# Kernel tuning notes

Measured on AMD Instinct MI355X. Metric: run time of the kernel, lower is better.

Reference implementation:

```python
import jax, jax.numpy as jnp
import numpy as np

LN_EPS = 1e-5      # torch nn.LayerNorm default
NORM_EPS = 1e-12   # torch F.normalize default


def _layer_norm(x, gamma, beta):
    mu = jnp.mean(x, axis=-1, keepdims=True)
    var = jnp.mean((x - mu) ** 2, axis=-1, keepdims=True)
    return (x - mu) * jax.lax.rsqrt(var + LN_EPS) * gamma + beta


def _l2_normalize_rows(w):
    n = jnp.sqrt(jnp.sum(w * w, axis=1, keepdims=True))
    return w / jnp.maximum(n, NORM_EPS)


def setup_inputs() -> dict:
    key = jax.random.key(0)
    B, D = 32768, 512
    ks = jax.random.split(key, 4)
    return {
        "stimulus": jax.random.normal(ks[0], (B, D), dtype=jnp.float32),
        "prev_activation": jax.random.normal(ks[1], (B, D), dtype=jnp.float32),
        "W": jax.random.normal(ks[2], (D, D), dtype=jnp.float32),
        "Wr": jax.random.normal(ks[3], (D, D), dtype=jnp.float32),
        "alpha": jnp.full((D,), 0.1, dtype=jnp.float32),
        "decay": jnp.full((D,), 0.01, dtype=jnp.float32),
        "ln_act_gamma": jnp.ones((D,), dtype=jnp.float32),
        "ln_act_beta": jnp.zeros((D,), dtype=jnp.float32),
        "ln_rec_gamma": jnp.ones((D,), dtype=jnp.float32),
        "ln_rec_beta": jnp.zeros((D,), dtype=jnp.float32),
    }


def reference(stimulus, prev_activation, W, Wr, alpha, decay,
              ln_act_gamma, ln_act_beta, ln_rec_gamma, ln_rec_beta):
    # recurrent path
    rec_out = prev_activation @ Wr                      # [B, D]
    rec_norm = _layer_norm(rec_out, ln_rec_gamma, ln_rec_beta)
    # stimulus path
    stim_out = stimulus @ W                             # [B, D]
    final = jax.nn.relu(stim_out + rec_norm)
    final = _layer_norm(final, ln_act_gamma, ln_act_beta)

    # Hebbian weight update (detached in the original module)
    heb_upd = jnp.einsum('bi,bj->ij', stimulus, stim_out) * alpha[None, :]
    rec_upd = jnp.einsum('bi,bj->ij', prev_activation, rec_out) * alpha[None, :]
    # diag(decay) @ W is a row-wise broadcast scale
    new_W = _l2_normalize_rows(W + heb_upd - decay[:, None] * W)
    new_Wr = _l2_normalize_rows(Wr + rec_upd - decay[:, None] * Wr)

    return final, new_W, new_Wr
```

## Files before the change

kernel.cpp:

```cpp
#include <hip/hip_runtime.h>
#include <stdint.h>

typedef unsigned int u32;
typedef unsigned short u16;
typedef float  f32x4 __attribute__((ext_vector_type(4)));
typedef u32    u32x4 __attribute__((ext_vector_type(4)));
typedef __bf16 bf16x8 __attribute__((ext_vector_type(8)));

static __device__ __forceinline__ u16 f2bf(float f){
  u32 u = __builtin_bit_cast(u32, f);
  return (u16)((u + 0x7FFFu + ((u >> 16) & 1u)) >> 16);
}

static __device__ __forceinline__ void async16(const void* g, void* l){
  __builtin_amdgcn_global_load_lds((const __attribute__((address_space(1))) u32*)g,
                                   (__attribute__((address_space(3))) u32*)l, 16, 0, 0);
}

static __device__ __forceinline__ float wave_sum(float v){
#pragma unroll
  for (int o = 32; o > 0; o >>= 1) v += __shfl_xor(v, o, 64);
  return v;
}

__global__ __launch_bounds__(256) void k_cvt(const float* __restrict__ s0, const float* __restrict__ s1,
                                             u16* __restrict__ d0, u16* __restrict__ d1){
  const float* __restrict__ src = blockIdx.y ? s1 : s0;
  u16* __restrict__ dst = blockIdx.y ? d1 : d0;
  size_t i = ((size_t)blockIdx.x*256 + threadIdx.x) * 8;
  f32x4 a = *(const f32x4*)(src + i);
  f32x4 b = *(const f32x4*)(src + i + 4);
  u32x4 w;
  w[0] = (u32)f2bf(a[0]) | ((u32)f2bf(a[1]) << 16);
  w[1] = (u32)f2bf(a[2]) | ((u32)f2bf(a[3]) << 16);
  w[2] = (u32)f2bf(b[0]) | ((u32)f2bf(b[1]) << 16);
  w[3] = (u32)f2bf(b[2]) | ((u32)f2bf(b[3]) << 16);
  *(u32x4*)(dst + i) = w;
}

__global__ __launch_bounds__(256) void k_tcvt(const float* __restrict__ s0, const float* __restrict__ s1,
                                              u16* __restrict__ d0, u16* __restrict__ d1,
                                              int R, int C){
  const float* __restrict__ src = blockIdx.z ? s1 : s0;
  u16* __restrict__ dst = blockIdx.z ? d1 : d0;
  __shared__ u16 lt[64*72];
  const int c0 = blockIdx.x * 64, r0 = blockIdx.y * 64;
  const int tid = threadIdx.x;
  const int rr = tid >> 4, c4 = tid & 15;
#pragma unroll
  for (int p = 0; p < 4; ++p){
    int r = rr + p*16;
    f32x4 f = *(const f32x4*)(src + (size_t)(r0 + r)*C + c0 + c4*4);
#pragma unroll
    for (int e = 0; e < 4; ++e) lt[(c4*4 + e)*72 + r] = f2bf(f[e]);
  }
  __syncthreads();
  const int c = tid >> 2, bg = tid & 3;
  const u32x4* lp = (const u32x4*)(lt + c*72 + bg*16);
  u32x4 w0 = lp[0], w1 = lp[1];
  u16* drow = dst + (size_t)(c0 + c)*R + r0 + bg*16;
  *(u32x4*)drow = w0;
  *(u32x4*)(drow + 8) = w1;
}

__global__ __launch_bounds__(512) void k_gemm_fwd(const u16* __restrict__ SN, const u16* __restrict__ PN,
                                                  const u16* __restrict__ Wt, const u16* __restrict__ Wrt,
                                                  u16* __restrict__ SO, u16* __restrict__ RO,
                                                  u16* __restrict__ SOT, u16* __restrict__ ROT){
  __shared__ char smem[67584];
  u16* sA = (u16*)smem;
  u16* sB = (u16*)(smem + 32768);
  const int tid = threadIdx.x;
  const int lane = tid & 63, wid = tid >> 6;
  const int wm = wid >> 1, wn = wid & 1;
  const int l15 = lane & 15, q = lane >> 4;
  const int id = blockIdx.x;
  const int c8 = id & 7, g = id >> 3;
  const int sel = g >> 6, h = g & 63;
  const int yb = c8*16 + (h >> 2), xb = h & 3;
  const int m0 = yb * 256, n0 = xb * 128;
  const u16* __restrict__ A  = sel ? PN  : SN;
  const u16* __restrict__ Bt = sel ? Wrt : Wt;
  u16* __restrict__ Cn = sel ? RO  : SO;
  u16* __restrict__ Ct = sel ? ROT : SOT;

  f32x4 acc[4][4];
  const f32x4 vzero = {0.f, 0.f, 0.f, 0.f};
#pragma unroll
  for (int a = 0; a < 4; ++a)
#pragma unroll
    for (int b = 0; b < 4; ++b) acc[a][b] = vzero;

#pragma unroll 1
  for (int kt = 0; kt < 8; ++kt){
    const int k0 = kt*64;
#pragma unroll
    for (int it = 0; it < 4; ++it){
      int gg0 = it*512 + tid;
      int r = gg0 >> 3, gp = gg0 & 7, gsw = gp ^ (r & 7);
      async16(A + (size_t)(m0 + r)*512 + k0 + gsw*8, (char*)sA + (size_t)gg0*16);
    }
#pragma unroll
    for (int it = 0; it < 2; ++it){
      int gg0 = it*512 + tid;
      int r = gg0 >> 3, gp = gg0 & 7, gsw = gp ^ (r & 7);
      async16(Bt + (size_t)(n0 + r)*512 + k0 + gsw*8, (char*)sB + (size_t)gg0*16);
    }
    __syncthreads();
#pragma unroll
    for (int kk = 0; kk < 2; ++kk){
      bf16x8 af[4], bfv[4];
#pragma unroll
      for (int mt = 0; mt < 4; ++mt){
        int r = wm*64 + mt*16 + l15;
        int gsw = (kk*4 + q) ^ (r & 7);
        af[mt] = *(const bf16x8*)(sA + (size_t)(r*8 + gsw)*8);
      }
#pragma unroll
      for (int nt = 0; nt < 4; ++nt){
        int r = wn*64 + nt*16 + l15;
        int gsw = (kk*4 + q) ^ (r & 7);
        bfv[nt] = *(const bf16x8*)(sB + (size_t)(r*8 + gsw)*8);
      }
#pragma unroll
      for (int mt = 0; mt < 4; ++mt)
#pragma unroll
        for (int nt = 0; nt < 4; ++nt)
          acc[mt][nt] = __builtin_amdgcn_mfma_f32_16x16x32_bf16(af[mt], bfv[nt], acc[mt][nt], 0, 0, 0);
    }
    __syncthreads();
  }

  u16* lt = (u16*)smem;
#pragma unroll
  for (int mt = 0; mt < 4; ++mt)
#pragma unroll
    for (int nt = 0; nt < 4; ++nt){
      f32x4 v = acc[mt][nt];
      u16 b0 = f2bf(v[0]), b1 = f2bf(v[1]), b2 = f2bf(v[2]), b3 = f2bf(v[3]);
      int n = wn*64 + nt*16 + l15;
      int mb = wm*64 + mt*16 + q*4;
      u16* cn = Cn + (size_t)(m0 + mb)*512 + n0 + n;
      cn[0] = b0; cn[512] = b1; cn[1024] = b2; cn[1536] = b3;
      *(u32*)(lt + n*264 + mb)     = (u32)b0 | ((u32)b1 << 16);
      *(u32*)(lt + n*264 + mb + 2) = (u32)b2 | ((u32)b3 << 16);
    }
  __syncthreads();
#pragma unroll
  for (int p = 0; p < 8; ++p){
    int gg0 = p*512 + tid;
    int n = gg0 >> 5, mg = gg0 & 31;
    u32x4 w = *(const u32x4*)(lt + n*264 + mg*8);
    *(u32x4*)(Ct + (size_t)(n0 + n)*32768 + m0 + mg*8) = w;
  }
}

__global__ __launch_bounds__(512) void k_gemm_upd(const u16* __restrict__ A0, const u16* __restrict__ B0,
                                                  const u16* __restrict__ A1, const u16* __restrict__ B1,
                                                  float* __restrict__ part){
  __shared__ char smem[67584];
  char* sAn = smem;
  u32*  sAt = (u32*)(smem + 16384);
  u16*  sB  = (u16*)(smem + 34816);
  const int tid = threadIdx.x;
  const int lane = tid & 63, wid = tid >> 6;
  const int wm = wid >> 2, wn = wid & 3;
  const int l15 = lane & 15, q = lane >> 4;
  const int id = blockIdx.x;
  const int c8 = id & 7, g = id >> 3;
  const int zz = c8*8 + (g >> 3);
  const int xy = g & 7;
  const int mat = zz >> 5, sp = zz & 31;
  const int yb = xy & 3, xb = xy >> 2;
  const u16* __restrict__ A = mat ? A1 : A0;
  const u16* __restrict__ B = mat ? B1 : B0;
  const int m0 = yb * 128, n0 = xb * 256;
  const int kb = sp * 1024;
  const int base_c = tid >> 5, pr = tid & 31;
  const int ce = (base_c + pr) & 15;

  f32x4 acc[4][4];
  const f32x4 vzero = {0.f, 0.f, 0.f, 0.f};
#pragma unroll
  for (int a = 0; a < 4; ++a)
#pragma unroll
    for (int b = 0; b < 4; ++b) acc[a][b] = vzero;

#pragma unroll 1
  for (int kt = 0; kt < 16; ++kt){
    const int k0 = kb + kt*64;
#pragma unroll
    for (int it = 0; it < 2; ++it){
      int gg0 = it*512 + tid;
      int r = gg0 >> 4, gp = gg0 & 15;
      async16(A + (size_t)(k0 + r)*512 + m0 + gp*8, sAn + (size_t)gg0*16);
    }
#pragma unroll
    for (int it = 0; it < 4; ++it){
      int gg0 = it*512 + tid;
      int r = gg0 >> 3, gp = gg0 & 7, gsw = gp ^ (r & 7);
      async16(B + (size_t)(n0 + r)*32768 + k0 + gsw*8, (char*)sB + (size_t)gg0*16);
    }
    __syncthreads();
    {
      u32x4 r0 = *(const u32x4*)(sAn + (size_t)(2*pr)*256 + ce*16);
      u32x4 r1 = *(const u32x4*)(sAn + (size_t)(2*pr)*256 + 256 + ce*16);
#pragma unroll
      for (int e = 0; e < 4; ++e){
        u32 lo = r0[e], hi = r1[e];
        sAt[(ce*8 + 2*e    )*36 + pr] = (lo & 0xFFFFu) | (hi << 16);
        sAt[(ce*8 + 2*e + 1)*36 + pr] = (lo >> 16) | (hi & 0xFFFF0000u);
      }
    }
    __syncthreads();
#pragma unroll
    for (int kk = 0; kk < 2; ++kk){
      bf16x8 af[4], bfv[4];
#pragma unroll
      for (int mt = 0; mt < 4; ++mt){
        int r = wm*64 + mt*16 + l15;
        af[mt] = *(const bf16x8*)(sAt + (size_t)r*36 + kk*16 + q*4);
      }
#pragma unroll
      for (int nt = 0; nt < 4; ++nt){
        int r = wn*64 + nt*16 + l15;
        int gsw = (kk*4 + q) ^ (r & 7);
        bfv[nt] = *(const bf16x8*)(sB + (size_t)(r*8 + gsw)*8);
      }
#pragma unroll
      for (int mt = 0; mt < 4; ++mt)
#pragma unroll
        for (int nt = 0; nt < 4; ++nt)
          acc[mt][nt] = __builtin_amdgcn_mfma_f32_16x16x32_bf16(af[mt], bfv[nt], acc[mt][nt], 0, 0, 0);
    }
    __syncthreads();
  }

  float* dst = part + (size_t)(mat*32 + sp)*262144;
#pragma unroll
  for (int mt = 0; mt < 4; ++mt)
#pragma unroll
    for (int nt = 0; nt < 4; ++nt){
      f32x4 v = acc[mt][nt];
      int n = wn*64 + nt*16 + l15;
      int mb = wm*64 + mt*16 + q*4;
      float* d = dst + (size_t)(m0 + mb)*512 + n0 + n;
      d[0] = v[0]; d[512] = v[1]; d[1024] = v[2]; d[1536] = v[3];
    }
}

__global__ __launch_bounds__(256) void k_ln(const u16* __restrict__ SO, const u16* __restrict__ RO,
                                            const float* __restrict__ ga, const float* __restrict__ ba,
                                            const float* __restrict__ gr, const float* __restrict__ br,
                                            float* __restrict__ out){
  const int wid = threadIdx.x >> 6, lane = threadIdx.x & 63;
  const size_t b = (size_t)blockIdx.x*4 + wid;
  const int c = lane*8;
  float x[8], t[8];
  {
    u32x4 u = *(const u32x4*)(RO + b*512 + c);
#pragma unroll
    for (int i = 0; i < 4; ++i){
      u32 w = u[i];
      x[2*i]   = __uint_as_float(w << 16);
      x[2*i+1] = __uint_as_float(w & 0xFFFF0000u);
    }
  }
  float s = 0.f, ss = 0.f;
#pragma unroll
  for (int e = 0; e < 8; ++e){ s += x[e]; ss += x[e]*x[e]; }
  s = wave_sum(s); ss = wave_sum(ss);
  float mu = s*(1.f/512.f);
  float var = fmaxf(ss*(1.f/512.f) - mu*mu, 0.f);
  float rs = rsqrtf(var + 1e-5f);
  f32x4 g0 = *(const f32x4*)(gr + c), g1 = *(const f32x4*)(gr + c + 4);
  f32x4 h0 = *(const f32x4*)(br + c), h1 = *(const f32x4*)(br + c + 4);
  {
    u32x4 u = *(const u32x4*)(SO + b*512 + c);
    float so[8];
#pragma unroll
    for (int i = 0; i < 4; ++i){
      u32 w = u[i];
      so[2*i]   = __uint_as_float(w << 16);
      so[2*i+1] = __uint_as_float(w & 0xFFFF0000u);
    }
#pragma unroll
    for (int e = 0; e < 4; ++e) t[e]   = fmaxf(so[e]   + (x[e]  -mu)*rs*g0[e] + h0[e], 0.f);
#pragma unroll
    for (int e = 0; e < 4; ++e) t[4+e] = fmaxf(so[4+e] + (x[4+e]-mu)*rs*g1[e] + h1[e], 0.f);
  }
  float s2 = 0.f, ss2 = 0.f;
#pragma unroll
  for (int e = 0; e < 8; ++e){ s2 += t[e]; ss2 += t[e]*t[e]; }
  s2 = wave_sum(s2); ss2 = wave_sum(ss2);
  float mu2 = s2*(1.f/512.f);
  float var2 = fmaxf(ss2*(1.f/512.f) - mu2*mu2, 0.f);
  float rs2 = rsqrtf(var2 + 1e-5f);
  f32x4 G0 = *(const f32x4*)(ga + c), G1 = *(const f32x4*)(ga + c + 4);
  f32x4 H0 = *(const f32x4*)(ba + c), H1 = *(const f32x4*)(ba + c + 4);
  f32x4 o0, o1;
#pragma unroll
  for (int e = 0; e < 4; ++e){
    o0[e] = (t[e]   - mu2)*rs2*G0[e] + H0[e];
    o1[e] = (t[4+e] - mu2)*rs2*G1[e] + H1[e];
  }
  *(f32x4*)(out + b*512 + c)     = o0;
  *(f32x4*)(out + b*512 + c + 4) = o1;
}

__global__ __launch_bounds__(256) void k_finalize(const float* __restrict__ W0, const float* __restrict__ W1,
                                                  const float* __restrict__ part,
                                                  const float* __restrict__ alpha, const float* __restrict__ decay,
                                                  float* __restrict__ out){
  const int i = blockIdx.x, mat = blockIdx.y;
  const int t = threadIdx.x;
  const float* Wm = mat ? W1 : W0;
  const float* pb = part + (size_t)mat*32*262144 + (size_t)i*512;
  const float dc = decay[i];
  float v[2], ssq = 0.f;
#pragma unroll
  for (int h = 0; h < 2; ++h){
    int j = t + h*256;
    float acc = 0.f;
#pragma unroll
    for (int sp = 0; sp < 32; ++sp) acc += pb[(size_t)sp*262144 + j];
    float val = Wm[(size_t)i*512 + j]*(1.f - dc) + alpha[j]*acc;
    v[h] = val; ssq += val*val;
  }
  float wsum = wave_sum(ssq);
  __shared__ float red[4];
  const int lane = t & 63, wid = t >> 6;
  if (lane == 0) red[wid] = wsum;
  __syncthreads();
  float tot = red[0] + red[1] + red[2] + red[3];
  float rn = 1.f / fmaxf(sqrtf(tot), 1e-12f);
  out[(size_t)mat*262144 + (size_t)i*512 + t]       = v[0]*rn;
  out[(size_t)mat*262144 + (size_t)i*512 + t + 256] = v[1]*rn;
}

extern "C" void kernel_launch(void* const* d_in, const int* in_sizes, int n_in,
                              void* d_out, int out_size, void* d_ws, size_t ws_size,
                              hipStream_t stream) {
  const float* S  = (const float*)d_in[0];
  const float* P  = (const float*)d_in[1];
  const float* W  = (const float*)d_in[2];
  const float* Wr = (const float*)d_in[3];
  const float* alpha = (const float*)d_in[4];
  const float* decay = (const float*)d_in[5];
  const float* ga = (const float*)d_in[6];
  const float* ba = (const float*)d_in[7];
  const float* gr = (const float*)d_in[8];
  const float* br = (const float*)d_in[9];
  float* out = (float*)d_out;

  char* ws = (char*)d_ws;
  u16* SN  = (u16*)(ws);
  u16* PN  = (u16*)(ws + 33554432);
  u16* SOT = (u16*)(ws + 67108864);
  u16* ROT = (u16*)(ws + 100663296);
  u16* SO  = (u16*)(ws + 134217728);
  u16* RO  = (u16*)(ws + 167772160);
  u16* Wt  = (u16*)(ws + 201326592);
  u16* Wrt = (u16*)(ws + 201850880);
  float* part = (float*)(ws + 134217728);

  k_cvt<<<dim3(8192, 2), dim3(256), 0, stream>>>(S, P, SN, PN);
  k_tcvt<<<dim3(8, 8, 2), dim3(256), 0, stream>>>(W, Wr, Wt, Wrt, 512, 512);
  k_gemm_fwd<<<dim3(1024), dim3(512), 0, stream>>>(SN, PN, Wt, Wrt, SO, RO, SOT, ROT);
  k_ln<<<dim3(8192), dim3(256), 0, stream>>>(SO, RO, ga, ba, gr, br, out);
  k_gemm_upd<<<dim3(512), dim3(512), 0, stream>>>(SN, SOT, PN, ROT, part);
  k_finalize<<<dim3(512, 2), dim3(256), 0, stream>>>(W, Wr, part, alpha, decay, out + 16777216);
}
```

Before: 317.5 us.

## Pre-transpose bf16 activations so the update GEMM skips its in-LDS transpose

The conversion kernel now also writes a transposed bf16 copy of stimulus and prev_activation when the workspace is large enough. If it is not, a separate transpose kernel produces that copy after the layernorm. The update GEMM then loads A tiles K-contiguous with the same XOR swizzle as B. This removes the per-tile LDS transpose pass and one barrier, and cuts LDS use. The cost is extra global traffic to write and read 64 MB of transposed activations, and the workspace layout is reorganised to fit both paths.

```diff
diff --git a/kernel.cpp b/kernel.cpp
--- a/kernel.cpp
+++ b/kernel.cpp
@@ -23,19 +23,71 @@
   return v;
 }
 
-__global__ __launch_bounds__(256) void k_cvt(const float* __restrict__ s0, const float* __restrict__ s1,
-                                             u16* __restrict__ d0, u16* __restrict__ d1){
-  const float* __restrict__ src = blockIdx.y ? s1 : s0;
-  u16* __restrict__ dst = blockIdx.y ? d1 : d0;
-  size_t i = ((size_t)blockIdx.x*256 + threadIdx.x) * 8;
-  f32x4 a = *(const f32x4*)(src + i);
-  f32x4 b = *(const f32x4*)(src + i + 4);
-  u32x4 w;
-  w[0] = (u32)f2bf(a[0]) | ((u32)f2bf(a[1]) << 16);
-  w[1] = (u32)f2bf(a[2]) | ((u32)f2bf(a[3]) << 16);
-  w[2] = (u32)f2bf(b[0]) | ((u32)f2bf(b[1]) << 16);
-  w[3] = (u32)f2bf(b[2]) | ((u32)f2bf(b[3]) << 16);
-  *(u32x4*)(dst + i) = w;
+__global__ __launch_bounds__(256) void k_cvt2(const float* __restrict__ s0, const float* __restrict__ s1,
+                                              u16* __restrict__ dn0, u16* __restrict__ dn1,
+                                              u16* __restrict__ dt0, u16* __restrict__ dt1,
+                                              int wn, int wt){
+  const float* __restrict__ src = blockIdx.z ? s1 : s0;
+  u16* __restrict__ dn = blockIdx.z ? dn1 : dn0;
+  u16* __restrict__ dt = blockIdx.z ? dt1 : dt0;
+  __shared__ u16 lt[64*72];
+  const int c0 = blockIdx.x * 64;
+  const int r0 = blockIdx.y * 64;
+  const int tid = threadIdx.x;
+  const int rr = tid >> 4, c4 = tid & 15;
+#pragma unroll
+  for (int p = 0; p < 4; ++p){
+    int r = rr + p*16;
+    f32x4 f = *(const f32x4*)(src + (size_t)(r0 + r)*512 + c0 + c4*4);
+    u16 b0 = f2bf(f[0]), b1 = f2bf(f[1]), b2 = f2bf(f[2]), b3 = f2bf(f[3]);
+    if (wt){
+      lt[(c4*4 + 0)*72 + r] = b0;
+      lt[(c4*4 + 1)*72 + r] = b1;
+      lt[(c4*4 + 2)*72 + r] = b2;
+      lt[(c4*4 + 3)*72 + r] = b3;
+    }
+    if (wn){
+      u32* qp = (u32*)(dn + (size_t)(r0 + r)*512 + c0 + c4*4);
+      qp[0] = (u32)b0 | ((u32)b1 << 16);
+      qp[1] = (u32)b2 | ((u32)b3 << 16);
+    }
+  }
+  if (!wt) return;
+  __syncthreads();
+  const int c = tid >> 2, bg = tid & 3;
+  const u32x4* lp = (const u32x4*)(lt + c*72 + bg*16);
+  u32x4 w0 = lp[0], w1 = lp[1];
+  u16* drow = dt + (size_t)(c0 + c)*32768 + r0 + bg*16;
+  *(u32x4*)drow = w0;
+  *(u32x4*)(drow + 8) = w1;
+}
+
+__global__ __launch_bounds__(256) void k_tpose(const u16* __restrict__ s0, const u16* __restrict__ s1,
+                                               u16* __restrict__ d0, u16* __restrict__ d1){
+  const u16* __restrict__ src = blockIdx.z ? s1 : s0;
+  u16* __restrict__ dst = blockIdx.z ? d1 : d0;
+  __shared__ u16 lt[64*72];
+  const int c0 = blockIdx.x * 64, r0 = blockIdx.y * 64;
+  const int tid = threadIdx.x;
+  const int rr = tid >> 3, c8 = tid & 7;
+#pragma unroll
+  for (int p = 0; p < 2; ++p){
+    int r = rr + p*32;
+    u32x4 w = *(const u32x4*)(src + (size_t)(r0 + r)*512 + c0 + c8*8);
+#pragma unroll
+    for (int e = 0; e < 4; ++e){
+      u32 v = w[e];
+      lt[(c8*8 + 2*e    )*72 + r] = (u16)(v & 0xFFFFu);
+      lt[(c8*8 + 2*e + 1)*72 + r] = (u16)(v >> 16);
+    }
+  }
+  __syncthreads();
+  const int c = tid >> 2, bg = tid & 3;
+  const u32x4* lp = (const u32x4*)(lt + c*72 + bg*16);
+  u32x4 w0 = lp[0], w1 = lp[1];
+  u16* drow = dst + (size_t)(c0 + c)*32768 + r0 + bg*16;
+  *(u32x4*)drow = w0;
+  *(u32x4*)(drow + 8) = w1;
 }
 
 __global__ __launch_bounds__(256) void k_tcvt(const float* __restrict__ s0, const float* __restrict__ s1,
@@ -158,10 +210,9 @@
 __global__ __launch_bounds__(512) void k_gemm_upd(const u16* __restrict__ A0, const u16* __restrict__ B0,
                                                   const u16* __restrict__ A1, const u16* __restrict__ B1,
                                                   float* __restrict__ part){
-  __shared__ char smem[67584];
-  char* sAn = smem;
-  u32*  sAt = (u32*)(smem + 16384);
-  u16*  sB  = (u16*)(smem + 34816);
+  __shared__ char smem[49152];
+  u16* sA = (u16*)smem;
+  u16* sB = (u16*)(smem + 16384);
   const int tid = threadIdx.x;
   const int lane = tid & 63, wid = tid >> 6;
   const int wm = wid >> 2, wn = wid & 3;
@@ -176,8 +227,6 @@
   const u16* __restrict__ B = mat ? B1 : B0;
   const int m0 = yb * 128, n0 = xb * 256;
   const int kb = sp * 1024;
-  const int base_c = tid >> 5, pr = tid & 31;
-  const int ce = (base_c + pr) & 15;
 
   f32x4 acc[4][4];
   const f32x4 vzero = {0.f, 0.f, 0.f, 0.f};
@@ -192,8 +241,8 @@
 #pragma unroll
     for (int it = 0; it < 2; ++it){
       int gg0 = it*512 + tid;
-      int r = gg0 >> 4, gp = gg0 & 15;
-      async16(A + (size_t)(k0 + r)*512 + m0 + gp*8, sAn + (size_t)gg0*16);
+      int r = gg0 >> 3, gp = gg0 & 7, gsw = gp ^ (r & 7);
+      async16(A + (size_t)(m0 + r)*32768 + k0 + gsw*8, (char*)sA + (size_t)gg0*16);
     }
 #pragma unroll
     for (int it = 0; it < 4; ++it){
@@ -202,24 +251,14 @@
       async16(B + (size_t)(n0 + r)*32768 + k0 + gsw*8, (char*)sB + (size_t)gg0*16);
     }
     __syncthreads();
-    {
-      u32x4 r0 = *(const u32x4*)(sAn + (size_t)(2*pr)*256 + ce*16);
-      u32x4 r1 = *(const u32x4*)(sAn + (size_t)(2*pr)*256 + 256 + ce*16);
-#pragma unroll
-      for (int e = 0; e < 4; ++e){
-        u32 lo = r0[e], hi = r1[e];
-        sAt[(ce*8 + 2*e    )*36 + pr] = (lo & 0xFFFFu) | (hi << 16);
-        sAt[(ce*8 + 2*e + 1)*36 + pr] = (lo >> 16) | (hi & 0xFFFF0000u);
-      }
-    }
-    __syncthreads();
 #pragma unroll
     for (int kk = 0; kk < 2; ++kk){
       bf16x8 af[4], bfv[4];
 #pragma unroll
       for (int mt = 0; mt < 4; ++mt){
         int r = wm*64 + mt*16 + l15;
-        af[mt] = *(const bf16x8*)(sAt + (size_t)r*36 + kk*16 + q*4);
+        int gsw = (kk*4 + q) ^ (r & 7);
+        af[mt] = *(const bf16x8*)(sA + (size_t)(r*8 + gsw)*8);
       }
 #pragma unroll
       for (int nt = 0; nt < 4; ++nt){
@@ -354,20 +393,41 @@
   float* out = (float*)d_out;
 
   char* ws = (char*)d_ws;
-  u16* SN  = (u16*)(ws);
-  u16* PN  = (u16*)(ws + 33554432);
-  u16* SOT = (u16*)(ws + 67108864);
-  u16* ROT = (u16*)(ws + 100663296);
-  u16* SO  = (u16*)(ws + 134217728);
-  u16* RO  = (u16*)(ws + 167772160);
-  u16* Wt  = (u16*)(ws + 201326592);
-  u16* Wrt = (u16*)(ws + 201850880);
-  float* part = (float*)(ws + 134217728);
-
-  k_cvt<<<dim3(8192, 2), dim3(256), 0, stream>>>(S, P, SN, PN);
+  const size_t M32 = 33554432;
+  const bool big = ws_size >= (size_t)269484032;
+
+  u16 *SN, *PN, *ST, *PT, *SOT, *ROT, *SO, *RO, *Wt, *Wrt;
+  if (big){
+    SN  = (u16*)(ws);
+    PN  = (u16*)(ws + 1*M32);
+    ST  = (u16*)(ws + 2*M32);
+    PT  = (u16*)(ws + 3*M32);
+    SOT = (u16*)(ws + 4*M32);
+    ROT = (u16*)(ws + 5*M32);
+    SO  = (u16*)(ws + 6*M32);
+    RO  = (u16*)(ws + 7*M32);
+    Wt  = (u16*)(ws + 8*M32);
+    Wrt = (u16*)(ws + 8*M32 + 524288);
+  } else {
+    SN  = (u16*)(ws);
+    PN  = (u16*)(ws + 1*M32);
+    SOT = (u16*)(ws + 2*M32);
+    ROT = (u16*)(ws + 3*M32);
+    SO  = (u16*)(ws + 4*M32);
+    RO  = (u16*)(ws + 5*M32);
+    Wt  = (u16*)(ws + 6*M32);
+    Wrt = (u16*)(ws + 6*M32 + 524288);
+    ST  = SO;
+    PT  = RO;
+  }
+  float* part = (float*)ws;
+
+  k_cvt2<<<dim3(8, 512, 2), dim3(256), 0, stream>>>(S, P, SN, PN, ST, PT, 1, big ? 1 : 0);
   k_tcvt<<<dim3(8, 8, 2), dim3(256), 0, stream>>>(W, Wr, Wt, Wrt, 512, 512);
   k_gemm_fwd<<<dim3(1024), dim3(512), 0, stream>>>(SN, PN, Wt, Wrt, SO, RO, SOT, ROT);
   k_ln<<<dim3(8192), dim3(256), 0, stream>>>(SO, RO, ga, ba, gr, br, out);
-  k_gemm_upd<<<dim3(512), dim3(512), 0, stream>>>(SN, SOT, PN, ROT, part);
+  if (!big)
+    k_tpose<<<dim3(8, 512, 2), dim3(256), 0, stream>>>(SN, PN, ST, PT);
+  k_gemm_upd<<<dim3(512), dim3(512), 0, stream>>>(ST, SOT, PT, ROT, part);
   k_finalize<<<dim3(512, 2), dim3(256), 0, stream>>>(W, Wr, part, alpha, decay, out + 16777216);
 }
```

After: 347.7 us. 9.5% more time.

## Fuse fp32-to-bf16 input conversion into both GEMM A-operand loads

Applied to the files above, without the earlier changes.

Removes the standalone conversion kernel for stimulus and prev_activation. Both GEMMs now load fp32 rows directly into registers, pack them to bf16 and store them to LDS. This avoids writing and re-reading bf16 copies of the large inputs and saves one launch. In exchange, the GEMMs read twice as many bytes per A tile, and the A operand no longer uses the direct global-to-LDS async path.

```diff
diff --git a/kernel.cpp b/kernel.cpp
--- a/kernel.cpp
+++ b/kernel.cpp
@@ -12,35 +12,28 @@
   return (u16)((u + 0x7FFFu + ((u >> 16) & 1u)) >> 16);
 }
 
-static __device__ __forceinline__ void async16(const void* g, void* l){
-  __builtin_amdgcn_global_load_lds((const __attribute__((address_space(1))) u32*)g,
-                                   (__attribute__((address_space(3))) u32*)l, 16, 0, 0);
-}
-
-static __device__ __forceinline__ float wave_sum(float v){
-#pragma unroll
-  for (int o = 32; o > 0; o >>= 1) v += __shfl_xor(v, o, 64);
-  return v;
-}
-
-__global__ __launch_bounds__(256) void k_cvt(const float* __restrict__ s0, const float* __restrict__ s1,
-                                             u16* __restrict__ d0, u16* __restrict__ d1){
-  const float* __restrict__ src = blockIdx.y ? s1 : s0;
-  u16* __restrict__ dst = blockIdx.y ? d1 : d0;
-  size_t i = ((size_t)blockIdx.x*256 + threadIdx.x) * 8;
-  f32x4 a = *(const f32x4*)(src + i);
-  f32x4 b = *(const f32x4*)(src + i + 4);
+static __device__ __forceinline__ u32x4 pack8(f32x4 a, f32x4 b){
   u32x4 w;
   w[0] = (u32)f2bf(a[0]) | ((u32)f2bf(a[1]) << 16);
   w[1] = (u32)f2bf(a[2]) | ((u32)f2bf(a[3]) << 16);
   w[2] = (u32)f2bf(b[0]) | ((u32)f2bf(b[1]) << 16);
   w[3] = (u32)f2bf(b[2]) | ((u32)f2bf(b[3]) << 16);
-  *(u32x4*)(dst + i) = w;
-}
-
-__global__ __launch_bounds__(256) void k_tcvt(const float* __restrict__ s0, const float* __restrict__ s1,
-                                              u16* __restrict__ d0, u16* __restrict__ d1,
-                                              int R, int C){
+  return w;
+}
+
+static __device__ __forceinline__ void async16(const void* g, void* l){
+  __builtin_amdgcn_global_load_lds((const __attribute__((address_space(1))) u32*)g,
+                                   (__attribute__((address_space(3))) u32*)l, 16, 0, 0);
+}
+
+static __device__ __forceinline__ float wave_sum(float v){
+#pragma unroll
+  for (int o = 32; o > 0; o >>= 1) v += __shfl_xor(v, o, 64);
+  return v;
+}
+
+__global__ __launch_bounds__(256) void k_wcvt(const float* __restrict__ s0, const float* __restrict__ s1,
+                                              u16* __restrict__ d0, u16* __restrict__ d1){
   const float* __restrict__ src = blockIdx.z ? s1 : s0;
   u16* __restrict__ dst = blockIdx.z ? d1 : d0;
   __shared__ u16 lt[64*72];
@@ -50,7 +43,7 @@
 #pragma unroll
   for (int p = 0; p < 4; ++p){
     int r = rr + p*16;
-    f32x4 f = *(const f32x4*)(src + (size_t)(r0 + r)*C + c0 + c4*4);
+    f32x4 f = *(const f32x4*)(src + (size_t)(r0 + r)*512 + c0 + c4*4);
 #pragma unroll
     for (int e = 0; e < 4; ++e) lt[(c4*4 + e)*72 + r] = f2bf(f[e]);
   }
@@ -58,12 +51,12 @@
   const int c = tid >> 2, bg = tid & 3;
   const u32x4* lp = (const u32x4*)(lt + c*72 + bg*16);
   u32x4 w0 = lp[0], w1 = lp[1];
-  u16* drow = dst + (size_t)(c0 + c)*R + r0 + bg*16;
+  u16* drow = dst + (size_t)(c0 + c)*512 + r0 + bg*16;
   *(u32x4*)drow = w0;
   *(u32x4*)(drow + 8) = w1;
 }
 
-__global__ __launch_bounds__(512) void k_gemm_fwd(const u16* __restrict__ SN, const u16* __restrict__ PN,
+__global__ __launch_bounds__(512) void k_gemm_fwd(const float* __restrict__ Sf, const float* __restrict__ Pf,
                                                   const u16* __restrict__ Wt, const u16* __restrict__ Wrt,
                                                   u16* __restrict__ SO, u16* __restrict__ RO,
                                                   u16* __restrict__ SOT, u16* __restrict__ ROT){
@@ -79,8 +72,8 @@
   const int sel = g >> 6, h = g & 63;
   const int yb = c8*16 + (h >> 2), xb = h & 3;
   const int m0 = yb * 256, n0 = xb * 128;
-  const u16* __restrict__ A  = sel ? PN  : SN;
-  const u16* __restrict__ Bt = sel ? Wrt : Wt;
+  const float* __restrict__ A = sel ? Pf  : Sf;
+  const u16* __restrict__ Bt  = sel ? Wrt : Wt;
   u16* __restrict__ Cn = sel ? RO  : SO;
   u16* __restrict__ Ct = sel ? ROT : SOT;
 
@@ -94,17 +87,25 @@
 #pragma unroll 1
   for (int kt = 0; kt < 8; ++kt){
     const int k0 = kt*64;
+    f32x4 fa[4], fb[4];
 #pragma unroll
     for (int it = 0; it < 4; ++it){
       int gg0 = it*512 + tid;
       int r = gg0 >> 3, gp = gg0 & 7, gsw = gp ^ (r & 7);
-      async16(A + (size_t)(m0 + r)*512 + k0 + gsw*8, (char*)sA + (size_t)gg0*16);
+      const float* src = A + (size_t)(m0 + r)*512 + k0 + gsw*8;
+      fa[it] = *(const f32x4*)src;
+      fb[it] = *(const f32x4*)(src + 4);
     }
 #pragma unroll
     for (int it = 0; it < 2; ++it){
       int gg0 = it*512 + tid;
       int r = gg0 >> 3, gp = gg0 & 7, gsw = gp ^ (r & 7);
       async16(Bt + (size_t)(n0 + r)*512 + k0 + gsw*8, (char*)sB + (size_t)gg0*16);
+    }
+#pragma unroll
+    for (int it = 0; it < 4; ++it){
+      int gg0 = it*512 + tid;
+      *(u32x4*)((char*)sA + (size_t)gg0*16) = pack8(fa[it], fb[it]);
     }
     __syncthreads();
 #pragma unroll
@@ -155,8 +156,8 @@
   }
 }
 
-__global__ __launch_bounds__(512) void k_gemm_upd(const u16* __restrict__ A0, const u16* __restrict__ B0,
-                                                  const u16* __restrict__ A1, const u16* __restrict__ B1,
+__global__ __launch_bounds__(512) void k_gemm_upd(const float* __restrict__ A0, const u16* __restrict__ B0,
+                                                  const float* __restrict__ A1, const u16* __restrict__ B1,
                                                   float* __restrict__ part){
   __shared__ char smem[67584];
   char* sAn = smem;
@@ -172,7 +173,7 @@
   const int xy = g & 7;
   const int mat = zz >> 5, sp = zz & 31;
   const int yb = xy & 3, xb = xy >> 2;
-  const u16* __restrict__ A = mat ? A1 : A0;
+  const float* __restrict__ A = mat ? A1 : A0;
   const u16* __restrict__ B = mat ? B1 : B0;
   const int m0 = yb * 128, n0 = xb * 256;
   const int kb = sp * 1024;
@@ -189,17 +190,25 @@
 #pragma unroll 1
   for (int kt = 0; kt < 16; ++kt){
     const int k0 = kb + kt*64;
+    f32x4 fa[2], fb[2];
 #pragma unroll
     for (int it = 0; it < 2; ++it){
       int gg0 = it*512 + tid;
       int r = gg0 >> 4, gp = gg0 & 15;
-      async16(A + (size_t)(k0 + r)*512 + m0 + gp*8, sAn + (size_t)gg0*16);
+      const float* src = A + (size_t)(k0 + r)*512 + m0 + gp*8;
+      fa[it] = *(const f32x4*)src;
+      fb[it] = *(const f32x4*)(src + 4);
     }
 #pragma unroll
     for (int it = 0; it < 4; ++it){
       int gg0 = it*512 + tid;
       int r = gg0 >> 3, gp = gg0 & 7, gsw = gp ^ (r & 7);
       async16(B + (size_t)(n0 + r)*32768 + k0 + gsw*8, (char*)sB + (size_t)gg0*16);
+    }
+#pragma unroll
+    for (int it = 0; it < 2; ++it){
+      int gg0 = it*512 + tid;
+      *(u32x4*)(sAn + (size_t)gg0*16) = pack8(fa[it], fb[it]);
     }
     __syncthreads();
     {
@@ -354,20 +363,17 @@
   float* out = (float*)d_out;
 
   char* ws = (char*)d_ws;
-  u16* SN  = (u16*)(ws);
-  u16* PN  = (u16*)(ws + 33554432);
-  u16* SOT = (u16*)(ws + 67108864);
-  u16* ROT = (u16*)(ws + 100663296);
-  u16* SO  = (u16*)(ws + 134217728);
-  u16* RO  = (u16*)(ws + 167772160);
-  u16* Wt  = (u16*)(ws + 201326592);
-  u16* Wrt = (u16*)(ws + 201850880);
-  float* part = (float*)(ws + 134217728);
-
-  k_cvt<<<dim3(8192, 2), dim3(256), 0, stream>>>(S, P, SN, PN);
-  k_tcvt<<<dim3(8, 8, 2), dim3(256), 0, stream>>>(W, Wr, Wt, Wrt, 512, 512);
-  k_gemm_fwd<<<dim3(1024), dim3(512), 0, stream>>>(SN, PN, Wt, Wrt, SO, RO, SOT, ROT);
+  u16* SOT = (u16*)(ws);
+  u16* ROT = (u16*)(ws + 33554432);
+  u16* SO  = (u16*)(ws + 67108864);
+  u16* RO  = (u16*)(ws + 100663296);
+  u16* Wt  = (u16*)(ws + 134217728);
+  u16* Wrt = (u16*)(ws + 134742016);
+  float* part = (float*)(ws + 67108864);
+
+  k_wcvt<<<dim3(8, 8, 2), dim3(256), 0, stream>>>(W, Wr, Wt, Wrt);
+  k_gemm_fwd<<<dim3(1024), dim3(512), 0, stream>>>(S, P, Wt, Wrt, SO, RO, SOT, ROT);
   k_ln<<<dim3(8192), dim3(256), 0, stream>>>(SO, RO, ga, ba, gr, br, out);
-  k_gemm_upd<<<dim3(512), dim3(512), 0, stream>>>(SN, SOT, PN, ROT, part);
+  k_gemm_upd<<<dim3(512), dim3(512), 0, stream>>>(S, SOT, P, ROT, part);
   k_finalize<<<dim3(512, 2), dim3(256), 0, stream>>>(W, Wr, part, alpha, decay, out + 16777216);
 }
```

Result: slower. 333.3 us (+5.0%).
